# Kernel optimization log

Hardware: AMD Instinct MI355X
Metric: run time of the kernel (lower is better)

## Reference

```python
import jax, jax.numpy as jnp
import numpy as np
import math

PH, PW = 14, 14      # patch size
DH, DW = 3, 3        # DCT block size
BINS = 256


def _dct_matrix(size: int) -> np.ndarray:
    m = np.zeros((size, size), dtype=np.float32)
    for i in range(size):
        for j in range(size):
            if i == 0:
                m[i, j] = math.sqrt(1.0 / size)
            else:
                m[i, j] = math.sqrt(2.0 / size) * math.cos(math.pi * (2 * j + 1) * i / (2 * size))
    return m


def setup_inputs() -> dict:
    key = jax.random.key(0)
    x = jax.random.uniform(key, (16, 3, 448, 448), dtype=jnp.float32)
    dct_matrix = jnp.asarray(_dct_matrix(DH))
    return {"x": x, "dct_matrix": dct_matrix}


def reference(x, dct_matrix):
    B, C, H, W = x.shape
    Hp, Wp = H // PH, W // PW
    # extract non-overlapping patches -> (B, Hp, Wp, C, PH, PW)
    patches = x.reshape(B, C, Hp, PH, Wp, PW).transpose(0, 2, 4, 1, 3, 5)

    # ---- per-patch pixel-value entropy (histogram via scatter-add) ----
    N = PH * PW
    pi = jnp.clip(jnp.round(jax.lax.stop_gradient(patches) * 255.0), 0, 255).astype(jnp.int32)
    flat = pi.reshape(-1, N)                       # (P, N), P = B*Hp*Wp*C
    P = flat.shape[0]
    counts = jnp.zeros((P, BINS), jnp.float32).at[jnp.arange(P)[:, None], flat].add(1.0)
    prob = counts / N + 1e-10
    entropy = -(prob * jnp.log2(prob)).sum(-1).reshape(B, Hp, Wp, C)

    # ---- sliding 3x3 windows inside each patch (stride 1) ----
    n = PH - DH + 1                                # 12 window positions per axis
    wins = jnp.stack(
        [patches[..., di:di + n, dj:dj + n] for di in range(DH) for dj in range(DW)],
        axis=-1,
    ).reshape(B, Hp, Wp, C, n, n, DH, DW)          # last two dims = within-window offsets

    # 2D DCT: D @ block @ D^T
    dct = jnp.einsum('ij,...jk,lk->...il', dct_matrix, wins, dct_matrix)

    # ---- direction variance of normalized stds ----
    S1 = jnp.std(dct, axis=-1).mean(-1)                       # rows
    S2 = jnp.std(dct, axis=-2).mean(-1)                       # cols
    S3 = jnp.std(jnp.diagonal(dct, axis1=-2, axis2=-1), axis=-1)
    S4 = jnp.std(jnp.diagonal(jnp.flip(dct, axis=-1), axis1=-2, axis2=-1), axis=-1)
    S = (S1 + S2 + S3 + S4) / 4.0 + 1e-8
    psi = jnp.var(jnp.stack([S1 / S, S2 / S, S3 / S, S4 / S], axis=-1), axis=-1, ddof=1)
    psi_m = psi.mean(axis=(-1, -2))                           # (B, Hp, Wp, C)

    richness = psi_m * entropy
    return richness.mean(-1)                                  # (B, Hp, Wp)
```

## Files before the change

kernel.cpp:

```cpp
#include <hip/hip_runtime.h>
#include <math.h>


typedef unsigned int uint32;

__device__ __forceinline__ float fsqrt_fast(float x) { return __builtin_amdgcn_sqrtf(x); }
__device__ __forceinline__ float frcp_fast(float x)  { return __builtin_amdgcn_rcpf(x);  }
__device__ __forceinline__ float flog2_fast(float x) { return __builtin_amdgcn_logf(x);  }

__device__ __forceinline__ float std3_fast(float a, float b, float c) {
    float s = a + b + c;
    float q = fmaf(a, a, fmaf(b, b, c * c));
    float v = fmaf(q, (1.0f / 3.0f), (s * s) * (-1.0f / 9.0f));
    return fsqrt_fast(fmaxf(v, 0.0f));
}

struct RunData {
    float2 a0, a1, a2, a3, b0, b1, b2, b3, c0, c1, c2, c3;
};

__device__ __forceinline__ RunData load_run(const float* base) {
    RunData r;
    r.a0 = *reinterpret_cast<const float2*>(base + 0);
    r.a1 = *reinterpret_cast<const float2*>(base + 2);
    r.a2 = *reinterpret_cast<const float2*>(base + 4);
    r.a3 = *reinterpret_cast<const float2*>(base + 6);
    r.b0 = *reinterpret_cast<const float2*>(base + 448);
    r.b1 = *reinterpret_cast<const float2*>(base + 450);
    r.b2 = *reinterpret_cast<const float2*>(base + 452);
    r.b3 = *reinterpret_cast<const float2*>(base + 454);
    r.c0 = *reinterpret_cast<const float2*>(base + 896);
    r.c1 = *reinterpret_cast<const float2*>(base + 898);
    r.c2 = *reinterpret_cast<const float2*>(base + 900);
    r.c3 = *reinterpret_cast<const float2*>(base + 902);
    return r;
}

__device__ __forceinline__ float run_psi(const RunData& rd, float k0, float k1, float k2) {
    float r0[8] = { rd.a0.x, rd.a0.y, rd.a1.x, rd.a1.y, rd.a2.x, rd.a2.y, rd.a3.x, rd.a3.y };
    float r1[8] = { rd.b0.x, rd.b0.y, rd.b1.x, rd.b1.y, rd.b2.x, rd.b2.y, rd.b3.x, rd.b3.y };
    float r2[8] = { rd.c0.x, rd.c0.y, rd.c1.x, rd.c1.y, rd.c2.x, rd.c2.y, rd.c3.x, rd.c3.y };

    float t0[8], t1[8], t2[8];
#pragma unroll
    for (int J = 0; J < 8; ++J) {
        float s = r0[J] + r2[J];
        t0[J] = k0 * (s + r1[J]);
        t1[J] = k1 * (r0[J] - r2[J]);
        t2[J] = k2 * fmaf(-2.0f, r1[J], s);
    }

    float psi_run = 0.0f;
#pragma unroll
    for (int m = 0; m < 6; ++m) {
        float X0 = t0[m],     X1 = t1[m],     X2 = t2[m];
        float Y0 = t0[m + 1], Y1 = t1[m + 1], Y2 = t2[m + 1];
        float Z0 = t0[m + 2], Z1 = t1[m + 2], Z2 = t2[m + 2];
        float xz0 = X0 + Z0, xz1 = X1 + Z1, xz2 = X2 + Z2;
        float d00 = k0 * (xz0 + Y0), d01 = k1 * (X0 - Z0), d02 = k2 * fmaf(-2.0f, Y0, xz0);
        float d10 = k0 * (xz1 + Y1), d11 = k1 * (X1 - Z1), d12 = k2 * fmaf(-2.0f, Y1, xz1);
        float d20 = k0 * (xz2 + Y2), d21 = k1 * (X2 - Z2), d22 = k2 * fmaf(-2.0f, Y2, xz2);

        float S1 = (std3_fast(d00, d01, d02) + std3_fast(d10, d11, d12) + std3_fast(d20, d21, d22)) * (1.0f / 3.0f);
        float S2 = (std3_fast(d00, d10, d20) + std3_fast(d01, d11, d21) + std3_fast(d02, d12, d22)) * (1.0f / 3.0f);
        float S3 = std3_fast(d00, d11, d22);
        float S4 = std3_fast(d02, d11, d20);

        float sumS = (S1 + S2) + (S3 + S4);
        float sumQ = fmaf(S1, S1, fmaf(S2, S2, fmaf(S3, S3, S4 * S4)));
        float h    = fmaxf(fmaf(-0.25f * sumS, sumS, sumQ), 0.0f);
        float Sm   = fmaf(sumS, 0.25f, 1e-8f);
        float inv  = frcp_fast(Sm);
        psi_run    = fmaf(h * inv * inv, (1.0f / 3.0f), psi_run);
    }
    return psi_run;
}

__global__ __launch_bounds__(192, 6) void richness_kernel(
    const float* __restrict__ x,
    const float* __restrict__ dctm,
    float* __restrict__ out)
{
    const int bid = blockIdx.x;
    const int wpg = bid & 3;
    const int hp  = (bid >> 2) & 31;
    const int b   = bid >> 7;
    const int tid = threadIdx.x;

    __shared__ uint32 hist[6][256];
    __shared__ float  psiPart[24][24];
    __shared__ float  entAcc[24];
    __shared__ float  richAcc[24];

    const float k0 = dctm[0];
    const float k1 = dctm[3];
    const float k2 = dctm[6];

    for (int i = tid; i < 6 * 256; i += 192) ((uint32*)hist)[i] = 0u;
    __syncthreads();

    int pcA[3], rrA[3];
    const float* rbase[3];
#pragma unroll
    for (int kr = 0; kr < 3; ++kr) {
        int rho = tid + 192 * kr;
        int pc  = rho / 24;
        int rr  = rho - pc * 24;
        pcA[kr] = pc; rrA[kr] = rr;
        int ch = pc >> 3, p = pc & 7;
        int wi = rr >> 1, half = rr & 1;
        rbase[kr] = x + (((size_t)(b * 3 + ch) * 448 + hp * 14 + wi) * 448)
                      + wpg * 112 + p * 14 + half * 6;
    }

#define HTASK(i, CH, COL, SRC) \
    int CH, COL; const float* SRC; { \
        int t_   = tid + 192 * (i); \
        CH       = t_ / 392;                   \
        int rem_ = t_ - CH * 392; \
        int row_ = rem_ / 28; \
        COL      = (rem_ - row_ * 28) * 4; \
        SRC      = x + (((size_t)(b * 3 + CH) * 448 + hp * 14 + row_) * 448) + wpg * 112 + COL; }

#define BIN4(V, CH, COL) { \
        _Pragma("unroll") \
        for (int e_ = 0; e_ < 4; ++e_) { \
            float val_ = (&(V).x)[e_]; \
            int bin_ = (int)rintf(val_ * 255.0f);    \
            bin_ = min(max(bin_, 0), 255); \
            int ce_ = (COL) + e_; \
            int p_  = (ce_ * 2341) >> 15;            \
            int pc_ = (CH) * 8 + p_; \
            atomicAdd(&hist[pc_ >> 2][bin_], 1u << ((pc_ & 3) * 8)); \
        }}

    HTASK(0, ch0, col0, src0) HTASK(1, ch1, col1, src1)
    HTASK(2, ch2, col2, src2) HTASK(3, ch3, col3, src3)
    HTASK(4, ch4, col4, src4) HTASK(5, ch5, col5, src5)

    RunData rd0 = load_run(rbase[0]);
    float4 h0 = *reinterpret_cast<const float4*>(src0);
    float4 h1 = *reinterpret_cast<const float4*>(src1);
    float psi0 = run_psi(rd0, k0, k1, k2);
    psiPart[pcA[0]][rrA[0]] = psi0;
    BIN4(h0, ch0, col0)
    BIN4(h1, ch1, col1)

    float4 h2 = *reinterpret_cast<const float4*>(src2);
    float4 h3 = *reinterpret_cast<const float4*>(src3);
    RunData rd1 = load_run(rbase[1]);
    float psi1 = run_psi(rd1, k0, k1, k2);
    psiPart[pcA[1]][rrA[1]] = psi1;
    BIN4(h2, ch2, col2)
    BIN4(h3, ch3, col3)

    float4 h4 = *reinterpret_cast<const float4*>(src4);
    float4 h5 = *reinterpret_cast<const float4*>(src5);
    RunData rd2 = load_run(rbase[2]);
    float psi2 = run_psi(rd2, k0, k1, k2);
    psiPart[pcA[2]][rrA[2]] = psi2;
    BIN4(h4, ch4, col4)
    BIN4(h5, ch5, col5)

    if (tid < 24) {
        int colT = (4 + tid) * 4;
        const float* srcT = x + (((size_t)(b * 3 + 2) * 448 + hp * 14 + 13) * 448) + wpg * 112 + colT;
        float4 hT = *reinterpret_cast<const float4*>(srcT);
        BIN4(hT, 2, colT)
    }
#undef HTASK
#undef BIN4
    __syncthreads();

    {
        const int pcE = tid >> 3, sub = tid & 7;
        const int rowW = pcE >> 2, sh = (pcE & 3) * 8;
        float negent = 0.0f;
#pragma unroll
        for (int kk = 0; kk < 32; ++kk) {
            uint32 c = (hist[rowW][sub + 8 * kk] >> sh) & 0xffu;
            float pr = (float)c * (1.0f / 196.0f) + 1e-10f;
            negent = fmaf(pr, flog2_fast(pr), negent);
        }
#pragma unroll
        for (int off = 1; off < 8; off <<= 1) negent += __shfl_xor(negent, off, 64);
        if (sub == 0) entAcc[pcE] = -negent;
    }
    __syncthreads();

    if (tid < 24) {
        float s = 0.0f;
#pragma unroll
        for (int r = 0; r < 24; ++r) s += psiPart[tid][r];
        richAcc[tid] = (s * (1.0f / 144.0f)) * entAcc[tid];
    }
    __syncthreads();

    if (tid < 8) {
        float rv = (richAcc[tid] + richAcc[8 + tid] + richAcc[16 + tid]) * (1.0f / 3.0f);
        out[(b * 32 + hp) * 32 + wpg * 8 + tid] = rv;
    }
}

extern "C" void kernel_launch(void* const* d_in, const int* in_sizes, int n_in,
                              void* d_out, int out_size, void* d_ws, size_t ws_size,
                              hipStream_t stream) {
    const float* x    = (const float*)d_in[0];
    const float* dctm = (const float*)d_in[1];
    float* out        = (float*)d_out;

    richness_kernel<<<2048, 192, 0, stream>>>(x, dctm, out);
}
```

Baseline: 38.60 us.

## Split work per channel into separate blocks and add a combine kernel

New measurement: 41.27 us. 6.9% more time.

```diff
diff --git a/kernel.cpp b/kernel.cpp
--- a/kernel.cpp
+++ b/kernel.cpp
@@ -76,6 +76,103 @@
     return psi_run;
 }
 
+#define BIN4_1CH(V, COL) { \
+        _Pragma("unroll") \
+        for (int e_ = 0; e_ < 4; ++e_) { \
+            float val_ = (&(V).x)[e_]; \
+            int bin_ = (int)rintf(val_ * 255.0f);    \
+            bin_ = min(max(bin_, 0), 255); \
+            int ce_ = (COL) + e_; \
+            int p_  = (ce_ * 2341) >> 15;            \
+            atomicAdd(&hist[p_ >> 2][bin_], 1u << ((p_ & 3) * 8)); \
+        }}
+
+__global__ __launch_bounds__(192, 8) void rich_pc_kernel(
+    const float* __restrict__ x,
+    const float* __restrict__ dctm,
+    float* __restrict__ ws)
+{
+    const int bid = blockIdx.x;
+    const int ch  = bid >> 11;
+    const int r_  = bid & 2047;
+    const int wpg = r_ & 3;
+    const int hp  = (r_ >> 2) & 31;
+    const int b   = r_ >> 7;
+    const int tid = threadIdx.x;
+
+    __shared__ uint32 hist[2][256];
+    __shared__ float  psiPart[8][24];
+    __shared__ float  entAcc[8];
+
+    const float k0 = dctm[0];
+    const float k1 = dctm[3];
+    const float k2 = dctm[6];
+
+    for (int i = tid; i < 512; i += 192) ((uint32*)hist)[i] = 0u;
+    __syncthreads();
+
+    const size_t plane = ((size_t)(b * 3 + ch) * 448 + hp * 14) * 448 + wpg * 112;
+
+    const int pl   = tid / 24;
+    const int rr   = tid - pl * 24;
+    const int wi   = rr >> 1, half = rr & 1;
+    const float* base = x + plane + (size_t)wi * 448 + pl * 14 + half * 6;
+
+    int row0 = tid / 28,  col0 = (tid - row0 * 28) * 4;
+    int t1_  = tid + 192;
+    int row1 = t1_ / 28,  col1 = (t1_ - row1 * 28) * 4;
+    const float* src0 = x + plane + (size_t)row0 * 448 + col0;
+    const float* src1 = x + plane + (size_t)row1 * 448 + col1;
+
+    RunData rd = load_run(base);
+    float4 h0 = *reinterpret_cast<const float4*>(src0);
+    float4 h1 = *reinterpret_cast<const float4*>(src1);
+
+    float psi = run_psi(rd, k0, k1, k2);
+    psiPart[pl][rr] = psi;
+
+    BIN4_1CH(h0, col0)
+    BIN4_1CH(h1, col1)
+    if (tid < 8) {
+        int colT = (20 + tid) * 4;
+        const float* srcT = x + plane + (size_t)13 * 448 + colT;
+        float4 hT = *reinterpret_cast<const float4*>(srcT);
+        BIN4_1CH(hT, colT)
+    }
+    __syncthreads();
+
+    if (tid < 64) {
+        const int pcE = tid >> 3, sub = tid & 7;
+        const int rowW = pcE >> 2, sh = (pcE & 3) * 8;
+        float negent = 0.0f;
+#pragma unroll
+        for (int kk = 0; kk < 32; ++kk) {
+            uint32 c = (hist[rowW][sub + 8 * kk] >> sh) & 0xffu;
+            float pr = (float)c * (1.0f / 196.0f) + 1e-10f;
+            negent = fmaf(pr, flog2_fast(pr), negent);
+        }
+#pragma unroll
+        for (int off = 1; off < 8; off <<= 1) negent += __shfl_xor(negent, off, 64);
+        if (sub == 0) entAcc[pcE] = -negent;
+    }
+    __syncthreads();
+
+    if (tid < 8) {
+        float s = 0.0f;
+#pragma unroll
+        for (int r = 0; r < 24; ++r) s += psiPart[tid][r];
+        ws[ch * 16384 + ((b * 32 + hp) * 32 + wpg * 8 + tid)] =
+            (s * (1.0f / 144.0f)) * entAcc[tid];
+    }
+}
+
+__global__ __launch_bounds__(256) void combine_kernel(
+    const float* __restrict__ ws, float* __restrict__ out)
+{
+    int i = blockIdx.x * 256 + threadIdx.x;
+    out[i] = (ws[i] + ws[16384 + i] + ws[32768 + i]) * (1.0f / 3.0f);
+}
+
 __global__ __launch_bounds__(192, 6) void richness_kernel(
     const float* __restrict__ x,
     const float* __restrict__ dctm,
@@ -99,76 +196,40 @@
     for (int i = tid; i < 6 * 256; i += 192) ((uint32*)hist)[i] = 0u;
     __syncthreads();
 
-    int pcA[3], rrA[3];
-    const float* rbase[3];
+#define BIN4(V, CH, COL) { \
+        _Pragma("unroll") \
+        for (int e_ = 0; e_ < 4; ++e_) { \
+            float val_ = (&(V).x)[e_]; \
+            int bin_ = (int)rintf(val_ * 255.0f); \
+            bin_ = min(max(bin_, 0), 255); \
+            int ce_ = (COL) + e_; \
+            int p_  = (ce_ * 2341) >> 15; \
+            int pc_ = (CH) * 8 + p_; \
+            atomicAdd(&hist[pc_ >> 2][bin_], 1u << ((pc_ & 3) * 8)); \
+        }}
+
+    for (int t = tid; t < 1176; t += 192) {
+        int ch  = t / 392;
+        int rem = t - ch * 392;
+        int row = rem / 28;
+        int col = (rem - row * 28) * 4;
+        const float* src = x + (((size_t)(b * 3 + ch) * 448 + hp * 14 + row) * 448) + wpg * 112 + col;
+        float4 v = *reinterpret_cast<const float4*>(src);
+        BIN4(v, ch, col)
+    }
+
 #pragma unroll
     for (int kr = 0; kr < 3; ++kr) {
         int rho = tid + 192 * kr;
         int pc  = rho / 24;
         int rr  = rho - pc * 24;
-        pcA[kr] = pc; rrA[kr] = rr;
         int ch = pc >> 3, p = pc & 7;
         int wi = rr >> 1, half = rr & 1;
-        rbase[kr] = x + (((size_t)(b * 3 + ch) * 448 + hp * 14 + wi) * 448)
-                      + wpg * 112 + p * 14 + half * 6;
-    }
-
-#define HTASK(i, CH, COL, SRC) \
-    int CH, COL; const float* SRC; { \
-        int t_   = tid + 192 * (i); \
-        CH       = t_ / 392;                   \
-        int rem_ = t_ - CH * 392; \
-        int row_ = rem_ / 28; \
-        COL      = (rem_ - row_ * 28) * 4; \
-        SRC      = x + (((size_t)(b * 3 + CH) * 448 + hp * 14 + row_) * 448) + wpg * 112 + COL; }
-
-#define BIN4(V, CH, COL) { \
-        _Pragma("unroll") \
-        for (int e_ = 0; e_ < 4; ++e_) { \
-            float val_ = (&(V).x)[e_]; \
-            int bin_ = (int)rintf(val_ * 255.0f);    \
-            bin_ = min(max(bin_, 0), 255); \
-            int ce_ = (COL) + e_; \
-            int p_  = (ce_ * 2341) >> 15;            \
-            int pc_ = (CH) * 8 + p_; \
-            atomicAdd(&hist[pc_ >> 2][bin_], 1u << ((pc_ & 3) * 8)); \
-        }}
-
-    HTASK(0, ch0, col0, src0) HTASK(1, ch1, col1, src1)
-    HTASK(2, ch2, col2, src2) HTASK(3, ch3, col3, src3)
-    HTASK(4, ch4, col4, src4) HTASK(5, ch5, col5, src5)
-
-    RunData rd0 = load_run(rbase[0]);
-    float4 h0 = *reinterpret_cast<const float4*>(src0);
-    float4 h1 = *reinterpret_cast<const float4*>(src1);
-    float psi0 = run_psi(rd0, k0, k1, k2);
-    psiPart[pcA[0]][rrA[0]] = psi0;
-    BIN4(h0, ch0, col0)
-    BIN4(h1, ch1, col1)
-
-    float4 h2 = *reinterpret_cast<const float4*>(src2);
-    float4 h3 = *reinterpret_cast<const float4*>(src3);
-    RunData rd1 = load_run(rbase[1]);
-    float psi1 = run_psi(rd1, k0, k1, k2);
-    psiPart[pcA[1]][rrA[1]] = psi1;
-    BIN4(h2, ch2, col2)
-    BIN4(h3, ch3, col3)
-
-    float4 h4 = *reinterpret_cast<const float4*>(src4);
-    float4 h5 = *reinterpret_cast<const float4*>(src5);
-    RunData rd2 = load_run(rbase[2]);
-    float psi2 = run_psi(rd2, k0, k1, k2);
-    psiPart[pcA[2]][rrA[2]] = psi2;
-    BIN4(h4, ch4, col4)
-    BIN4(h5, ch5, col5)
-
-    if (tid < 24) {
-        int colT = (4 + tid) * 4;
-        const float* srcT = x + (((size_t)(b * 3 + 2) * 448 + hp * 14 + 13) * 448) + wpg * 112 + colT;
-        float4 hT = *reinterpret_cast<const float4*>(srcT);
-        BIN4(hT, 2, colT)
-    }
-#undef HTASK
+        const float* base = x + (((size_t)(b * 3 + ch) * 448 + hp * 14 + wi) * 448)
+                              + wpg * 112 + p * 14 + half * 6;
+        RunData rd = load_run(base);
+        psiPart[pc][rr] = run_psi(rd, k0, k1, k2);
+    }
 #undef BIN4
     __syncthreads();
 
@@ -209,5 +270,11 @@
     const float* dctm = (const float*)d_in[1];
     float* out        = (float*)d_out;
 
-    richness_kernel<<<2048, 192, 0, stream>>>(x, dctm, out);
-}
+    if (ws_size >= 49152 * sizeof(float) && d_ws != nullptr) {
+        float* ws = (float*)d_ws;
+        rich_pc_kernel<<<6144, 192, 0, stream>>>(x, dctm, ws);
+        combine_kernel<<<64, 256, 0, stream>>>(ws, out);
+    } else {
+        richness_kernel<<<2048, 192, 0, stream>>>(x, dctm, out);
+    }
+}
```
